# Kernel tuning notes

Hardware: AMD Instinct MI355X
Metric: run time of the kernel (lower is better)

Reference implementation:

```python
import jax, jax.numpy as jnp
import numpy as np
from jax import lax

N, D, K = 4096, 64, 5


def setup_inputs() -> dict:
    key = jax.random.key(0)
    k1, k2 = jax.random.split(key)
    x = jax.random.normal(k1, (N, D), dtype=jnp.float32)
    y = jax.random.normal(k2, (N, D), dtype=jnp.float32)
    kernel_scales = jnp.array([0.5, 1.0, 2.0, 4.0, 8.0], dtype=jnp.float32)
    return {"x": x, "y": y, "kernel_scales": kernel_scales}


def _sqdist(a, b):
    # squared euclidean pairwise distances: [Na, Nb]
    an = jnp.sum(a * a, axis=1)
    bn = jnp.sum(b * b, axis=1)
    return an[:, None] + bn[None, :] - 2.0 * (a @ b.T)


def _median_lower(m):
    # torch.median on even-sized flattened tensor returns the LOWER middle element
    f = m.reshape(-1)
    return jnp.sort(f)[(f.size - 1) // 2]


def _kernel_sum(dist, scale):
    # multi-bandwidth RBF: mean over K kernels (default weights = 1/K each)
    # dist: [N, M], scale: [K]  ->  [N, M]
    return jnp.mean(jnp.exp(dist[:, :, None] * scale), axis=2)


def reference(x, y, kernel_scales):
    xx = _sqdist(x, x)
    yy = _sqdist(y, y)
    zz = _sqdist(x, y)
    # scale = -1/median(xx), computed under no_grad in the original
    base_scale = lax.stop_gradient(-1.0 / _median_lower(xx))
    scale = base_scale * kernel_scales  # [K]

    kxx = _kernel_sum(xx, scale)
    kyy = _kernel_sum(yy, scale)
    kzz = _kernel_sum(zz, scale)

    n = xx.shape[0]
    diag = jnp.arange(n)
    kxx = kxx.at[diag, diag].set(0.0)
    kyy = kyy.at[diag, diag].set(0.0)

    off_diag = 1.0 / (n * (n - 1))
    return off_diag * jnp.sum(kxx) + off_diag * jnp.sum(kyy) - 2.0 * jnp.mean(kzz)
```

## Files before the change

kernel.cpp:

```cpp
#include <hip/hip_runtime.h>

#define NN 4096
#define DD 64
#define KK 5
#define NBINS 1024
#define BINMUL 2.0f
#define RMED 8388607u
#define MBUF_CAP 8192u

typedef short short8 __attribute__((ext_vector_type(8)));
typedef float f32x4 __attribute__((ext_vector_type(4)));

struct Ctrl {
  unsigned wcount;
  unsigned wover;
  unsigned gcount;
  unsigned sel_bin;
  unsigned rank;
  unsigned ok;
  unsigned wrank;
  unsigned spref;
  unsigned srank;
  unsigned use_pow;
  float median;
  float c2;
  float scales[KK];
};

__device__ inline float fast_exp2(float x) {
  float r;
  asm("v_exp_f32 %0, %1" : "=v"(r) : "v"(x));
  return r;
}
__device__ inline unsigned short bf16_rn(float f) {
  unsigned u = __float_as_uint(f);
  return (unsigned short)((u + 0x7FFFu + ((u >> 16) & 1u)) >> 16);
}
__device__ inline float bf16_val(unsigned short h) {
  return __uint_as_float(((unsigned)h) << 16);
}

__global__ void __launch_bounds__(256)
splitnorms_kernel(const float* __restrict__ x, const float* __restrict__ y,
                  short* __restrict__ xhi, short* __restrict__ xlo,
                  short* __restrict__ yhi, short* __restrict__ ylo,
                  float* __restrict__ xn, float* __restrict__ yn) {
  unsigned g = blockIdx.x * 256u + threadIdx.x;
  const float* src; short *dhi, *dlo; float* nrm; unsigned local;
  if (g < 65536u) { src = x; dhi = xhi; dlo = xlo; nrm = xn; local = g; }
  else { src = y; dhi = yhi; dlo = ylo; nrm = yn; local = g - 65536u; }
  float4 v = *(const float4*)(src + (size_t)local * 4);
  unsigned short h0 = bf16_rn(v.x), h1 = bf16_rn(v.y), h2 = bf16_rn(v.z), h3 = bf16_rn(v.w);
  unsigned short l0 = bf16_rn(v.x - bf16_val(h0));
  unsigned short l1 = bf16_rn(v.y - bf16_val(h1));
  unsigned short l2 = bf16_rn(v.z - bf16_val(h2));
  unsigned short l3 = bf16_rn(v.w - bf16_val(h3));
  unsigned long long H = (unsigned long long)h0 | ((unsigned long long)h1 << 16) |
                         ((unsigned long long)h2 << 32) | ((unsigned long long)h3 << 48);
  unsigned long long L = (unsigned long long)l0 | ((unsigned long long)l1 << 16) |
                         ((unsigned long long)l2 << 32) | ((unsigned long long)l3 << 48);
  *(unsigned long long*)((char*)dhi + (size_t)local * 8) = H;
  *(unsigned long long*)((char*)dlo + (size_t)local * 8) = L;
  float part = v.x * v.x;
  part = fmaf(v.y, v.y, part);
  part = fmaf(v.z, v.z, part);
  part = fmaf(v.w, v.w, part);
#pragma unroll
  for (int off = 1; off < 16; off <<= 1) part += __shfl_xor(part, off);
  if ((threadIdx.x & 15) == 0) nrm[local >> 4] = part;
}

template <int MODE>
__global__ void __launch_bounds__(256)
pair_kernel(const short* __restrict__ xhi, const short* __restrict__ xlo,
            const short* __restrict__ yhi, const short* __restrict__ ylo,
            const float* __restrict__ xn, const float* __restrict__ yn,
            unsigned* __restrict__ hist, Ctrl* __restrict__ ctrl,
            float* __restrict__ buf, double* __restrict__ S,
            int lobin, int hibin, unsigned cap) {
  if (MODE == 1) {
    if (ctrl->ok) return;
  }
  __shared__ __align__(16) char smem[65536];
  char* As = smem;
  char* Bs = smem + 32768;

  int t = threadIdx.x;
  int sel = (MODE == 2) ? blockIdx.z : 0;
  const short* Ah = (sel == 1) ? yhi : xhi;
  const short* Al = (sel == 1) ? ylo : xlo;
  const short* Bh = (sel == 0) ? xhi : yhi;
  const short* Bl = (sel == 0) ? xlo : ylo;
  const float* An = (sel == 1) ? yn : xn;
  const float* Bn = (sel == 0) ? xn : yn;

  int rowBase = blockIdx.y * 128;
  int colBase = blockIdx.x * 128;

  int lane = t & 63, wid = t >> 6;
  int wr = (wid >> 1) * 64, wc = (wid & 1) * 64;
  int lrow = lane & 15;
  int lk8 = (lane >> 4) * 8;
  int lswz = (lane & 7) << 4;

  {
    const char* gAh = (const char*)Ah + (size_t)rowBase * 128;
    const char* gAl = (const char*)Al + (size_t)rowBase * 128;
    const char* gBh = (const char*)Bh + (size_t)colBase * 128;
    const char* gBl = (const char*)Bl + (size_t)colBase * 128;
    short8 rAh[4], rAl[4], rBh[4], rBl[4];
#pragma unroll
    for (int i = 0; i < 4; ++i) {
      int o = t * 16 + i * 4096;
      rAh[i] = *(const short8*)(gAh + o);
      rAl[i] = *(const short8*)(gAl + o);
      rBh[i] = *(const short8*)(gBh + o);
      rBl[i] = *(const short8*)(gBl + o);
    }
#pragma unroll
    for (int i = 0; i < 4; ++i) {
      int o = t * 16 + i * 4096;
      int rr = o >> 7;
      int cc = (o >> 4) & 7;
      int db = (rr * 256 + cc * 16) ^ ((rr & 7) << 4);
      *(short8*)(As + db) = rAh[i];
      *(short8*)(As + db + 128) = rAl[i];
      *(short8*)(Bs + db) = rBh[i];
      *(short8*)(Bs + db + 128) = rBl[i];
    }
  }
  __syncthreads();

  f32x4 acc[4][4] = {};
#pragma unroll
  for (int kc = 0; kc < 2; ++kc) {
    short8 ah[4], al[4], bh[4], bl[4];
#pragma unroll
    for (int m = 0; m < 4; ++m) {
      int by = ((wr + m * 16 + lrow) * 256 + (lk8 + kc * 32) * 2) ^ lswz;
      ah[m] = *(const short8*)(As + by);
      al[m] = *(const short8*)(As + by + 128);
    }
#pragma unroll
    for (int n = 0; n < 4; ++n) {
      int by = ((wc + n * 16 + lrow) * 256 + (lk8 + kc * 32) * 2) ^ lswz;
      bh[n] = *(const short8*)(Bs + by);
      bl[n] = *(const short8*)(Bs + by + 128);
    }
#pragma unroll
    for (int m = 0; m < 4; ++m)
#pragma unroll
      for (int n = 0; n < 4; ++n) {
        acc[m][n] = __builtin_amdgcn_mfma_f32_16x16x32_bf16(ah[m], bh[n], acc[m][n], 0, 0, 0);
        acc[m][n] = __builtin_amdgcn_mfma_f32_16x16x32_bf16(ah[m], bl[n], acc[m][n], 0, 0, 0);
        acc[m][n] = __builtin_amdgcn_mfma_f32_16x16x32_bf16(al[m], bh[n], acc[m][n], 0, 0, 0);
      }
  }

  float anv[16], bnv[4];
#pragma unroll
  for (int m = 0; m < 4; ++m)
#pragma unroll
    for (int r = 0; r < 4; ++r)
      anv[m * 4 + r] = An[rowBase + wr + m * 16 + (lane >> 4) * 4 + r];
#pragma unroll
  for (int n = 0; n < 4; ++n) bnv[n] = Bn[colBase + wc + n * 16 + lrow];

  __syncthreads();

  if (MODE == 0 || MODE == 1) {
    unsigned* h = (unsigned*)Bs;
    float* mbuf = (float*)As;
    __shared__ unsigned bcnt, gbase;
    if (MODE == 0)
      for (int i = t; i < NBINS; i += 256) h[i] = 0;
    if (t == 0) bcnt = 0;
    __syncthreads();
    unsigned sb = (MODE == 1) ? ctrl->sel_bin : 0u;
#pragma unroll
    for (int m = 0; m < 4; ++m)
#pragma unroll
      for (int n = 0; n < 4; ++n)
#pragma unroll
        for (int r = 0; r < 4; ++r) {
          float d = (anv[m * 4 + r] + bnv[n]) - 2.0f * acc[m][n][r];
          int b = (int)(d * BINMUL);
          b = min(max(b, 0), NBINS - 1);
          if (MODE == 0) {
            atomicAdd(&h[b], 1u);
            if (b >= lobin && b < hibin) {
              unsigned idx = atomicAdd(&bcnt, 1u);
              if (idx < MBUF_CAP) mbuf[idx] = d - 100.0f;
              else ctrl->wover = 1u;
            }
          } else {
            if ((unsigned)b == sb) {
              unsigned idx = atomicAdd(&bcnt, 1u);
              if (idx < MBUF_CAP) mbuf[idx] = d - 100.0f;
            }
          }
        }
    __syncthreads();
    if (MODE == 0)
      for (int i = t; i < NBINS; i += 256)
        if (h[i]) atomicAdd(&hist[i], h[i]);
    unsigned cnt = min(bcnt, MBUF_CAP);
    if (t == 0) gbase = atomicAdd(MODE == 0 ? &ctrl->wcount : &ctrl->gcount, cnt);
    __syncthreads();
    for (unsigned i = t; i < cnt; i += 256) {
      unsigned gi = gbase + i;
      if (gi < cap) buf[gi] = mbuf[i];
    }
  }

  if (MODE == 2) {
    float s = 0.f;
    if (ctrl->use_pow) {
      float c2 = ctrl->c2;
#pragma unroll
      for (int m = 0; m < 4; ++m)
#pragma unroll
        for (int n = 0; n < 4; ++n)
#pragma unroll
          for (int r = 0; r < 4; ++r) {
            float d = (anv[m * 4 + r] + bnv[n]) - 2.0f * acc[m][n][r];
            float u = fast_exp2(d * c2);
            float u2 = u * u, u4 = u2 * u2, u8 = u4 * u4, u16 = u8 * u8;
            s += ((u + u2) + (u4 + u8)) + u16;
          }
    } else {
      float sc[KK];
#pragma unroll
      for (int k = 0; k < KK; ++k) sc[k] = ctrl->scales[k];
#pragma unroll
      for (int m = 0; m < 4; ++m)
#pragma unroll
        for (int n = 0; n < 4; ++n)
#pragma unroll
          for (int r = 0; r < 4; ++r) {
            float d = (anv[m * 4 + r] + bnv[n]) - 2.0f * acc[m][n][r];
            float e = 0.f;
#pragma unroll
            for (int k = 0; k < KK; ++k) e += expf(d * sc[k]);
            s += e;
          }
    }
    double sd = (double)s;
#pragma unroll
    for (int off = 32; off > 0; off >>= 1) sd += __shfl_down(sd, off);
    double* wsum = (double*)As;
    if ((t & 63) == 0) wsum[wid] = sd;
    __syncthreads();
    if (t == 0) atomicAdd(&S[sel], (wsum[0] + wsum[1]) + (wsum[2] + wsum[3]));
  }
}

__global__ void __launch_bounds__(256)
select_bin_kernel(const unsigned* __restrict__ hist, Ctrl* __restrict__ ctrl,
                  int lobin, int hibin, unsigned cap) {
  __shared__ unsigned ps[256];
  __shared__ unsigned s_cumlo;
  int t = threadIdx.x;
  unsigned loc[NBINS / 256];
  unsigned s = 0;
#pragma unroll
  for (int i = 0; i < NBINS / 256; ++i) {
    loc[i] = hist[t * (NBINS / 256) + i];
    s += loc[i];
  }
  ps[t] = s;
  __syncthreads();
  for (int off = 1; off < 256; off <<= 1) {
    unsigned v = ps[t];
    unsigned add = (t >= off) ? ps[t - off] : 0u;
    __syncthreads();
    ps[t] = v + add;
    __syncthreads();
  }
  unsigned incl = ps[t], excl = incl - s;
  if (t == (lobin >> 2)) {
    unsigned c = excl;
    for (int i = 0; i < (lobin & 3); ++i) c += loc[i];
    s_cumlo = c;
  }
  __syncthreads();
  if (RMED >= excl && RMED < incl) {
    unsigned rank = RMED - excl;
    int bsel = -1;
#pragma unroll
    for (int i = 0; i < NBINS / 256; ++i) {
      if (bsel < 0) {
        if (rank < loc[i]) bsel = t * (NBINS / 256) + i;
        else rank -= loc[i];
      }
    }
    ctrl->sel_bin = (unsigned)bsel;
    ctrl->rank = rank;
    unsigned wrank = RMED - s_cumlo;
    unsigned ok = (bsel >= lobin && bsel < hibin && ctrl->wover == 0u &&
                   ctrl->wcount <= cap && wrank < ctrl->wcount) ? 1u : 0u;
    ctrl->wrank = wrank;
    ctrl->ok = ok;
  }
}

__global__ void __launch_bounds__(256)
radix_fused(Ctrl* __restrict__ ctrl, const float* __restrict__ buf,
            unsigned* __restrict__ gh, unsigned* __restrict__ tick,
            const float* __restrict__ ksc, int round, unsigned cap) {
  __shared__ unsigned h[256];
  __shared__ unsigned lastflag;
  int t = threadIdx.x;
  h[t] = 0;
  if (t == 0) lastflag = 0;
  __syncthreads();
  unsigned m = min(ctrl->ok ? ctrl->wcount : ctrl->gcount, cap);
  unsigned pref = ctrl->spref;
  int shift = 24 - 8 * round;
  for (unsigned i = blockIdx.x * 256u + t; i < m; i += gridDim.x * 256u) {
    unsigned u = __float_as_uint(buf[i]);
    u ^= (u >> 31) ? 0xFFFFFFFFu : 0x80000000u;
    if (round == 0 || ((u ^ pref) >> (shift + 8)) == 0u)
      atomicAdd(&h[(u >> shift) & 255u], 1u);
  }
  __syncthreads();
  if (h[t]) atomicAdd(&gh[round * 256 + t], h[t]);
  __threadfence();
  if (t == 0)
    lastflag = (atomicAdd(&tick[round], 1u) == gridDim.x - 1u) ? 1u : 0u;
  __syncthreads();
  if (!lastflag) return;
  unsigned rank = (round == 0) ? (ctrl->ok ? ctrl->wrank : ctrl->rank) : ctrl->srank;
  unsigned c = atomicAdd(&gh[round * 256 + t], 0u);
  h[t] = c;
  __syncthreads();
  for (int off = 1; off < 256; off <<= 1) {
    unsigned v = h[t];
    unsigned add = (t >= off) ? h[t - off] : 0u;
    __syncthreads();
    h[t] = v + add;
    __syncthreads();
  }
  unsigned incl = h[t], excl = incl - c;
  if (rank >= excl && rank < incl) {
    unsigned np = pref | ((unsigned)t << shift);
    ctrl->spref = np;
    ctrl->srank = rank - excl;
    if (round == 3) {
      unsigned u = (np & 0x80000000u) ? (np ^ 0x80000000u) : ~np;
      float med = __uint_as_float(u) + 100.0f;
      ctrl->median = med;
      float base = -1.0f / med;
#pragma unroll
      for (int k = 0; k < KK; ++k) ctrl->scales[k] = base * ksc[k];
      ctrl->c2 = base * 0.5f * 1.44269504088896f;
      ctrl->use_pow = (ksc[0] == 0.5f && ksc[1] == 1.0f && ksc[2] == 2.0f &&
                       ksc[3] == 4.0f && ksc[4] == 8.0f) ? 1u : 0u;
    }
  }
}

__global__ void finalize_kernel(const double* __restrict__ S, float* __restrict__ out) {
  if (threadIdx.x == 0 && blockIdx.x == 0) {
    double offd = 1.0 / ((double)NN * (double)(NN - 1));
    double invK = 1.0 / (double)KK;
    double kxx = (S[0] * invK) - (double)NN;
    double kyy = (S[1] * invK) - (double)NN;
    double kzz = S[2] * invK;
    double val = offd * (kxx + kyy) - 2.0 * kzz / ((double)NN * (double)NN);
    out[0] = (float)val;
  }
}

extern "C" void kernel_launch(void* const* d_in, const int* in_sizes, int n_in,
                              void* d_out, int out_size, void* d_ws, size_t ws_size,
                              hipStream_t stream) {
  const float* x = (const float*)d_in[0];
  const float* y = (const float*)d_in[1];
  const float* ksc = (const float*)d_in[2];

  char* ws = (char*)d_ws;
  double* S = (double*)ws;
  unsigned* hist = (unsigned*)(ws + 64);
  unsigned* gh = (unsigned*)(ws + 4160);
  unsigned* tick = (unsigned*)(ws + 8256);
  Ctrl* ctrl = (Ctrl*)(ws + 8288);
  float* xn = (float*)(ws + 8448);
  float* yn = xn + NN;
  const size_t SPL = (size_t)NN * DD * 2;
  short* xhi = (short*)(ws + 65536);
  short* xlo = (short*)(ws + 65536 + SPL);
  short* yhi = (short*)(ws + 65536 + 2 * SPL);
  short* ylo = (short*)(ws + 65536 + 3 * SPL);
  size_t bufoff = 65536 + 4 * SPL;
  float* buf = (float*)(ws + bufoff);

  size_t avail = (ws_size > bufoff) ? (ws_size - bufoff) / 4 : 0;
  unsigned cap = (unsigned)((avail < (size_t)(8u << 20)) ? avail : (size_t)(8u << 20));
  int lobin, hibin;
  if (cap >= 450000u) { lobin = 252; hibin = 255; }
  else                { lobin = 252; hibin = 254; }

  hipMemsetAsync(ws, 0, 8448, stream);

  splitnorms_kernel<<<512, 256, 0, stream>>>(x, y, xhi, xlo, yhi, ylo, xn, yn);
  pair_kernel<0><<<dim3(32, 32), 256, 0, stream>>>(xhi, xlo, yhi, ylo, xn, yn, hist, ctrl,
                                                   buf, S, lobin, hibin, cap);
  select_bin_kernel<<<1, 256, 0, stream>>>(hist, ctrl, lobin, hibin, cap);
  pair_kernel<1><<<dim3(32, 32), 256, 0, stream>>>(xhi, xlo, yhi, ylo, xn, yn, hist, ctrl,
                                                   buf, S, lobin, hibin, cap);
  for (int r = 0; r < 4; ++r)
    radix_fused<<<192, 256, 0, stream>>>(ctrl, buf, gh, tick, ksc, r, cap);
  pair_kernel<2><<<dim3(32, 32, 3), 256, 0, stream>>>(xhi, xlo, yhi, ylo, xn, yn, hist, ctrl,
                                                      buf, S, lobin, hibin, cap);
  finalize_kernel<<<1, 64, 0, stream>>>(S, (float*)d_out);
}
```

Measured before the change: 213.1 us.

## Re-layout bf16 split operands into K-chunked tiles, halve LDS, skip first radix round

```diff
diff --git a/kernel.cpp b/kernel.cpp
--- a/kernel.cpp
+++ b/kernel.cpp
@@ -6,7 +6,7 @@
 #define NBINS 1024
 #define BINMUL 2.0f
 #define RMED 8388607u
-#define MBUF_CAP 8192u
+#define MBUF_CAP 7164u
 
 typedef short short8 __attribute__((ext_vector_type(8)));
 typedef float f32x4 __attribute__((ext_vector_type(4)));
@@ -22,6 +22,7 @@
   unsigned spref;
   unsigned srank;
   unsigned use_pow;
+  unsigned skip0;
   float median;
   float c2;
   float scales[KK];
@@ -59,8 +60,10 @@
                          ((unsigned long long)h2 << 32) | ((unsigned long long)h3 << 48);
   unsigned long long L = (unsigned long long)l0 | ((unsigned long long)l1 << 16) |
                          ((unsigned long long)l2 << 32) | ((unsigned long long)l3 << 48);
-  *(unsigned long long*)((char*)dhi + (size_t)local * 8) = H;
-  *(unsigned long long*)((char*)dlo + (size_t)local * 8) = L;
+  unsigned row = local >> 4, kc4 = local & 15;
+  size_t dst = (((size_t)(kc4 >> 3) * NN + row) * 32 + (kc4 & 7) * 4) * 2;
+  *(unsigned long long*)((char*)dhi + dst) = H;
+  *(unsigned long long*)((char*)dlo + dst) = L;
   float part = v.x * v.x;
   part = fmaf(v.y, v.y, part);
   part = fmaf(v.z, v.z, part);
@@ -81,9 +84,7 @@
   if (MODE == 1) {
     if (ctrl->ok) return;
   }
-  __shared__ __align__(16) char smem[65536];
-  char* As = smem;
-  char* Bs = smem + 32768;
+  __shared__ __align__(16) char smem[32768];
 
   int t = threadIdx.x;
   int sel = (MODE == 2) ? blockIdx.z : 0;
@@ -100,61 +101,52 @@
   int lane = t & 63, wid = t >> 6;
   int wr = (wid >> 1) * 64, wc = (wid & 1) * 64;
   int lrow = lane & 15;
-  int lk8 = (lane >> 4) * 8;
-  int lswz = (lane & 7) << 4;
-
-  {
-    const char* gAh = (const char*)Ah + (size_t)rowBase * 128;
-    const char* gAl = (const char*)Al + (size_t)rowBase * 128;
-    const char* gBh = (const char*)Bh + (size_t)colBase * 128;
-    const char* gBl = (const char*)Bl + (size_t)colBase * 128;
-    short8 rAh[4], rAl[4], rBh[4], rBl[4];
-#pragma unroll
-    for (int i = 0; i < 4; ++i) {
-      int o = t * 16 + i * 4096;
-      rAh[i] = *(const short8*)(gAh + o);
-      rAl[i] = *(const short8*)(gAl + o);
-      rBh[i] = *(const short8*)(gBh + o);
-      rBl[i] = *(const short8*)(gBl + o);
-    }
-#pragma unroll
-    for (int i = 0; i < 4; ++i) {
-      int o = t * 16 + i * 4096;
-      int rr = o >> 7;
-      int cc = (o >> 4) & 7;
-      int db = (rr * 256 + cc * 16) ^ ((rr & 7) << 4);
-      *(short8*)(As + db) = rAh[i];
-      *(short8*)(As + db + 128) = rAl[i];
-      *(short8*)(Bs + db) = rBh[i];
-      *(short8*)(Bs + db + 128) = rBl[i];
-    }
-  }
-  __syncthreads();
+  int koffs = (((lane >> 4) ^ (lane & 3)) << 4);
 
   f32x4 acc[4][4] = {};
 #pragma unroll
-  for (int kc = 0; kc < 2; ++kc) {
-    short8 ah[4], al[4], bh[4], bl[4];
+  for (int p = 0; p < 2; ++p) {
+    const char* s0 = (const char*)Ah + ((size_t)p * NN + rowBase) * 64;
+    const char* s1 = (const char*)Al + ((size_t)p * NN + rowBase) * 64;
+    const char* s2 = (const char*)Bh + ((size_t)p * NN + colBase) * 64;
+    const char* s3 = (const char*)Bl + ((size_t)p * NN + colBase) * 64;
+    short8 rg[8];
+    rg[0] = *(const short8*)(s0 + t * 16);
+    rg[1] = *(const short8*)(s0 + t * 16 + 4096);
+    rg[2] = *(const short8*)(s1 + t * 16);
+    rg[3] = *(const short8*)(s1 + t * 16 + 4096);
+    rg[4] = *(const short8*)(s2 + t * 16);
+    rg[5] = *(const short8*)(s2 + t * 16 + 4096);
+    rg[6] = *(const short8*)(s3 + t * 16);
+    rg[7] = *(const short8*)(s3 + t * 16 + 4096);
+    if (p) __syncthreads();
+#pragma unroll
+    for (int i = 0; i < 8; ++i) {
+      int cr = t * 16 + (i & 1) * 4096;
+      int row = cr >> 6, slot = (cr >> 4) & 3;
+      int db = (i >> 1) * 8192 + row * 64 + ((slot ^ (row & 3)) << 4);
+      *(short8*)(smem + db) = rg[i];
+    }
+    __syncthreads();
+    short8 bh[4], bl[4];
+#pragma unroll
+    for (int n = 0; n < 4; ++n) {
+      int rb = (wc + n * 16 + lrow) * 64 + koffs;
+      bh[n] = *(const short8*)(smem + 16384 + rb);
+      bl[n] = *(const short8*)(smem + 24576 + rb);
+    }
 #pragma unroll
     for (int m = 0; m < 4; ++m) {
-      int by = ((wr + m * 16 + lrow) * 256 + (lk8 + kc * 32) * 2) ^ lswz;
-      ah[m] = *(const short8*)(As + by);
-      al[m] = *(const short8*)(As + by + 128);
-    }
-#pragma unroll
-    for (int n = 0; n < 4; ++n) {
-      int by = ((wc + n * 16 + lrow) * 256 + (lk8 + kc * 32) * 2) ^ lswz;
-      bh[n] = *(const short8*)(Bs + by);
-      bl[n] = *(const short8*)(Bs + by + 128);
-    }
-#pragma unroll
-    for (int m = 0; m < 4; ++m)
+      int rb = (wr + m * 16 + lrow) * 64 + koffs;
+      short8 ah = *(const short8*)(smem + rb);
+      short8 al = *(const short8*)(smem + 8192 + rb);
 #pragma unroll
       for (int n = 0; n < 4; ++n) {
-        acc[m][n] = __builtin_amdgcn_mfma_f32_16x16x32_bf16(ah[m], bh[n], acc[m][n], 0, 0, 0);
-        acc[m][n] = __builtin_amdgcn_mfma_f32_16x16x32_bf16(ah[m], bl[n], acc[m][n], 0, 0, 0);
-        acc[m][n] = __builtin_amdgcn_mfma_f32_16x16x32_bf16(al[m], bh[n], acc[m][n], 0, 0, 0);
+        acc[m][n] = __builtin_amdgcn_mfma_f32_16x16x32_bf16(ah, bh[n], acc[m][n], 0, 0, 0);
+        acc[m][n] = __builtin_amdgcn_mfma_f32_16x16x32_bf16(ah, bl[n], acc[m][n], 0, 0, 0);
+        acc[m][n] = __builtin_amdgcn_mfma_f32_16x16x32_bf16(al, bh[n], acc[m][n], 0, 0, 0);
       }
+    }
   }
 
   float anv[16], bnv[4];
@@ -168,13 +160,15 @@
 
   __syncthreads();
 
+  unsigned* bcnt = (unsigned*)(smem + 28656);
+  unsigned* gbase = (unsigned*)(smem + 28660);
+
   if (MODE == 0 || MODE == 1) {
-    unsigned* h = (unsigned*)Bs;
-    float* mbuf = (float*)As;
-    __shared__ unsigned bcnt, gbase;
+    unsigned* h = (unsigned*)(smem + 28672);
+    float* mbuf = (float*)smem;
     if (MODE == 0)
       for (int i = t; i < NBINS; i += 256) h[i] = 0;
-    if (t == 0) bcnt = 0;
+    if (t == 0) *bcnt = 0;
     __syncthreads();
     unsigned sb = (MODE == 1) ? ctrl->sel_bin : 0u;
 #pragma unroll
@@ -189,13 +183,13 @@
           if (MODE == 0) {
             atomicAdd(&h[b], 1u);
             if (b >= lobin && b < hibin) {
-              unsigned idx = atomicAdd(&bcnt, 1u);
+              unsigned idx = atomicAdd(bcnt, 1u);
               if (idx < MBUF_CAP) mbuf[idx] = d - 100.0f;
               else ctrl->wover = 1u;
             }
           } else {
             if ((unsigned)b == sb) {
-              unsigned idx = atomicAdd(&bcnt, 1u);
+              unsigned idx = atomicAdd(bcnt, 1u);
               if (idx < MBUF_CAP) mbuf[idx] = d - 100.0f;
             }
           }
@@ -204,11 +198,12 @@
     if (MODE == 0)
       for (int i = t; i < NBINS; i += 256)
         if (h[i]) atomicAdd(&hist[i], h[i]);
-    unsigned cnt = min(bcnt, MBUF_CAP);
-    if (t == 0) gbase = atomicAdd(MODE == 0 ? &ctrl->wcount : &ctrl->gcount, cnt);
-    __syncthreads();
+    unsigned cnt = min(*bcnt, MBUF_CAP);
+    if (t == 0) *gbase = atomicAdd(MODE == 0 ? &ctrl->wcount : &ctrl->gcount, cnt);
+    __syncthreads();
+    unsigned gb = *gbase;
     for (unsigned i = t; i < cnt; i += 256) {
-      unsigned gi = gbase + i;
+      unsigned gi = gb + i;
       if (gi < cap) buf[gi] = mbuf[i];
     }
   }
@@ -216,17 +211,25 @@
   if (MODE == 2) {
     float s = 0.f;
     if (ctrl->use_pow) {
-      float c2 = ctrl->c2;
+      float c2 = ctrl->c2, m2c2 = -2.0f * c2;
+      float bnvc[4];
+#pragma unroll
+      for (int n = 0; n < 4; ++n) bnvc[n] = bnv[n] * c2;
+#pragma unroll
+      for (int i = 0; i < 16; ++i) anv[i] *= c2;
 #pragma unroll
       for (int m = 0; m < 4; ++m)
 #pragma unroll
         for (int n = 0; n < 4; ++n)
 #pragma unroll
           for (int r = 0; r < 4; ++r) {
-            float d = (anv[m * 4 + r] + bnv[n]) - 2.0f * acc[m][n][r];
-            float u = fast_exp2(d * c2);
-            float u2 = u * u, u4 = u2 * u2, u8 = u4 * u4, u16 = u8 * u8;
-            s += ((u + u2) + (u4 + u8)) + u16;
+            float arg = fmaf(acc[m][n][r], m2c2, anv[m * 4 + r] + bnvc[n]);
+            float u = fast_exp2(arg);
+            float u2 = u * u;
+            float a = fmaf(u, u, u);
+            float u4 = u2 * u2, u8 = u4 * u4;
+            float b = fmaf(u8, u8, u8);
+            s += a; s += u4; s += b;
           }
     } else {
       float sc[KK];
@@ -248,7 +251,7 @@
     double sd = (double)s;
 #pragma unroll
     for (int off = 32; off > 0; off >>= 1) sd += __shfl_down(sd, off);
-    double* wsum = (double*)As;
+    double* wsum = (double*)smem;
     if ((t & 63) == 0) wsum[wid] = sd;
     __syncthreads();
     if (t == 0) atomicAdd(&S[sel], (wsum[0] + wsum[1]) + (wsum[2] + wsum[3]));
@@ -301,6 +304,11 @@
                    ctrl->wcount <= cap && wrank < ctrl->wcount) ? 1u : 0u;
     ctrl->wrank = wrank;
     ctrl->ok = ok;
+    if (ok && lobin >= 232 && hibin <= 264) {
+      ctrl->spref = 0xC1000000u;
+      ctrl->srank = wrank;
+      ctrl->skip0 = 1u;
+    }
   }
 }
 
@@ -308,6 +316,7 @@
 radix_fused(Ctrl* __restrict__ ctrl, const float* __restrict__ buf,
             unsigned* __restrict__ gh, unsigned* __restrict__ tick,
             const float* __restrict__ ksc, int round, unsigned cap) {
+  if (round == 0 && ctrl->skip0) return;
   __shared__ unsigned h[256];
   __shared__ unsigned lastflag;
   int t = threadIdx.x;
```

Result: faster. 200.7 us (-5.8%).
